# Kernel tuning notes

Measured on AMD Instinct MI355X. Metric: run time of the kernel, lower is better.

## Reference

```python
import jax, jax.numpy as jnp
import numpy as np

LAYERS, BLOCKS = 10, 4
RC, DC, SC, EC, CLASSES = 32, 32, 256, 256, 256
KS = 2
OUTPUT_LENGTH = 4096


def _dilations():
    ds = []
    init = 1
    for _b in range(BLOCKS):
        nd = 1
        for _i in range(LAYERS):
            ds.append((nd, init))
            init = nd
            nd *= 2
    return ds

DILATIONS = _dilations()


def dilate(x, dilation, init_dilation):
    # Faithful port of pytorch-wavenet dilate(): folds time into batch (or back)
    # by the ratio dilation/init_dilation, front-padding with zeros if needed.
    n, c, l = x.shape
    if dilation == init_dilation:
        return x
    if dilation > init_dilation:
        r = dilation // init_dilation
        new_l = -(-l // r) * r  # ceil to multiple of r
        if new_l != l:
            x = jnp.pad(x, ((0, 0), (0, 0), (new_l - l, 0)))  # pad_start=True
            l = new_l
        l_new, n_new = l // r, n * r
    else:
        r = init_dilation // dilation
        l_new, n_new = l * r, n // r
    x = jnp.transpose(x, (1, 2, 0)).reshape(c, l_new, n_new)  # (c, l, n) view
    return jnp.transpose(x, (2, 0, 1))


def conv2tap(x, w):
    # valid Conv1d, kernel_size=2, no bias; x: [n,c,l], w: [o,c,2]
    return jax.lax.conv_general_dilated(x, w, (1,), 'VALID',
                                        dimension_numbers=('NCH', 'OIH', 'NCH'))


def conv1x1(x, w):
    # 1x1 Conv1d as einsum; x: [n,c,l], w: [o,c]
    return jnp.einsum('ncl,oc->nol', x, w)


def setup_inputs() -> dict:
    key = jax.random.key(0)
    ks = jax.random.split(key, 10)
    nl = LAYERS * BLOCKS
    s = 0.05
    return {
        'x_input': jax.random.normal(ks[0], (8, CLASSES, 16384), jnp.float32),
        'start_w': jax.random.normal(ks[1], (RC, CLASSES, 1), jnp.float32) * s,
        'filter_w': jax.random.normal(ks[2], (nl, DC, RC, KS), jnp.float32) * s,
        'gate_w': jax.random.normal(ks[3], (nl, DC, RC, KS), jnp.float32) * s,
        'residual_w': jax.random.normal(ks[4], (nl, RC, DC, 1), jnp.float32) * s,
        'skip_w': jax.random.normal(ks[5], (nl, SC, DC, 1), jnp.float32) * s,
        'end1_w': jax.random.normal(ks[6], (EC, SC, 1), jnp.float32) * s,
        'end1_b': jnp.zeros((EC,), jnp.float32),
        'end2_w': jax.random.normal(ks[7], (CLASSES, EC, 1), jnp.float32) * s,
        'end2_b': jnp.zeros((CLASSES,), jnp.float32),
    }


def reference(x_input, start_w, filter_w, gate_w, residual_w, skip_w,
              end1_w, end1_b, end2_w, end2_b):
    x = conv1x1(x_input, start_w[:, :, 0])
    x_skip = None
    for i, (d, d0) in enumerate(DILATIONS):
        xr = dilate(x, d, d0)
        f = jnp.tanh(conv2tap(xr, filter_w[i]))
        g = jax.nn.sigmoid(conv2tap(xr, gate_w[i]))
        x = f * g
        xs = dilate(x, 1, d) if x.shape[2] != 1 else x
        # NOTE: the source never reassigns `skip`, so its try/except always
        # falls to the except branch and only the LAST layer's skip survives.
        x_skip = conv1x1(xs, skip_w[i][:, :, 0])
        x = conv1x1(x, residual_w[i][:, :, 0]) + xr[:, :, KS - 1:]
    y = jax.nn.relu(x_skip)
    y = jax.nn.relu(conv1x1(y, end1_w[:, :, 0]) + end1_b[None, :, None])
    y = conv1x1(y, end2_w[:, :, 0]) + end2_b[None, :, None]
    n, c, _l = y.shape
    y = y[:, :, -OUTPUT_LENGTH:]
    return jnp.transpose(y, (0, 2, 1)).reshape(n * OUTPUT_LENGTH, c)
```

## Files before the change

kernel.cpp:

```cpp
#include <hip/hip_runtime.h>
#include <hip/hip_bf16.h>
#include <math.h>


#define TS   8192
#define T0   8188
#define NB   8
#define RCH  32
#define CLS  256
#define TOUT 4096

#define OFF_WBLOB 0
#define OFF_ST    204800
#define OFF_SK    212992
#define OFF_E1T   221184
#define OFF_E2T   286720
#define OFF_XA    352256
#define OFF_XB    (OFF_XA + NB*RCH*TS)
#define OFF_H1    (OFF_XB + NB*RCH*TS)
#define OFF_E1    (OFF_H1 + NB*256*TOUT)

__device__ __forceinline__ float tanh_fast(float x) {
    float e = __expf(2.0f * x);
    return 1.0f - 2.0f / (e + 1.0f);
}
__device__ __forceinline__ float sigmoid_fast(float x) {
    return 1.0f / (1.0f + __expf(-x));
}

__global__ void repack_kernel(const float* __restrict__ start_w,
                              const float* __restrict__ filter_w,
                              const float* __restrict__ gate_w,
                              const float* __restrict__ residual_w,
                              const float* __restrict__ skip_w,
                              const float* __restrict__ end1_w,
                              const float* __restrict__ end2_w,
                              float* __restrict__ ws) {
    int id = blockIdx.x * 256 + threadIdx.x;
    if (id < 204800) {
        int l = id / 5120, r = id % 5120;
        float v;
        if (r < 4096) {
            const float* src = (r < 2048) ? filter_w : gate_w;
            int rr = r & 2047;
            int ic = rr >> 6, k = (rr >> 5) & 1, oc = rr & 31;
            v = src[((l * 32 + oc) * 32 + ic) * 2 + k];
        } else {
            int rr = r - 4096;
            int ic = rr >> 5, oc = rr & 31;
            v = residual_w[(l * 32 + oc) * 32 + ic];
        }
        ws[OFF_WBLOB + id] = v;
    } else if (id < 204800 + 8192) {
        int r = id - 204800;
        int ic = r >> 5, oc = r & 31;
        ws[OFF_ST + r] = start_w[oc * 256 + ic];
    } else if (id < 212992 + 8192) {
        int r = id - 212992;
        int dc = r >> 8, sc = r & 255;
        ws[OFF_SK + r] = skip_w[(39 * 256 + sc) * 32 + dc];
    } else if (id < 221184 + 65536) {
        int r = id - 221184;
        int sc = r >> 8, ec = r & 255;
        ws[OFF_E1T + r] = end1_w[ec * 256 + sc];
    } else if (id < 286720 + 65536) {
        int r = id - 286720;
        int ec = r >> 8, cc = r & 255;
        ws[OFF_E2T + r] = end2_w[cc * 256 + ec];
    }
}

__global__ __launch_bounds__(256) void start_kernel(const float* __restrict__ xin,
                                                    const float* __restrict__ st,
                                                    float* __restrict__ xout) {
    int t = blockIdx.x * 256 + threadIdx.x;
    int og = blockIdx.y;
    int b = blockIdx.z;
    if (t >= T0) return;
    const float* xi = xin + (size_t)b * 256 * 16384 + (16384 - T0) + t;
    const float* wb = st + og * 16;
    float acc[16];
#pragma unroll
    for (int c = 0; c < 16; c++) acc[c] = 0.f;
#pragma unroll 4
    for (int ic = 0; ic < 256; ic++) {
        float xv = xi[ic * 16384];
        const float* w = wb + ic * 32;
#pragma unroll
        for (int c = 0; c < 16; c++) acc[c] = fmaf(w[c], xv, acc[c]);
    }
    float* xo = xout + ((size_t)(b * RCH) + og * 16) * TS + t;
#pragma unroll
    for (int c = 0; c < 16; c++) xo[c * TS] = acc[c];
}

__global__ __launch_bounds__(256) void layer_kernel(const float* __restrict__ xin,
                                                    float* __restrict__ xout,
                                                    const float* __restrict__ wl,
                                                    int d, int Tout) {
    __shared__ float hs[32][64];
    int tx = threadIdx.x;
    int cg = __builtin_amdgcn_readfirstlane(threadIdx.y);
    int t  = blockIdx.x * 64 + tx;
    int b  = blockIdx.y;
    bool act = (t < Tout);

    const float* xi = xin + (size_t)(b * RCH) * TS + t;
    const float* wf = wl +        cg * 8;
    const float* wg = wl + 2048 + cg * 8;
    const float* wr = wl + 4096 + cg * 8;

    float accf[8], accg[8];
#pragma unroll
    for (int j = 0; j < 8; j++) { accf[j] = 0.f; accg[j] = 0.f; }

#pragma unroll 4
    for (int ic = 0; ic < 32; ic++) {
        float a = xi[ic * TS];
        float c = xi[ic * TS + d];
        const float* w0 = wf + ic * 64;
        const float* w1 = wg + ic * 64;
#pragma unroll
        for (int j = 0; j < 8; j++) accf[j] = fmaf(w0[j],      a, accf[j]);
#pragma unroll
        for (int j = 0; j < 8; j++) accf[j] = fmaf(w0[32 + j], c, accf[j]);
#pragma unroll
        for (int j = 0; j < 8; j++) accg[j] = fmaf(w1[j],      a, accg[j]);
#pragma unroll
        for (int j = 0; j < 8; j++) accg[j] = fmaf(w1[32 + j], c, accg[j]);
    }

#pragma unroll
    for (int j = 0; j < 8; j++)
        hs[cg * 8 + j][tx] = tanh_fast(accf[j]) * sigmoid_fast(accg[j]);
    __syncthreads();

    float accr[8];
#pragma unroll
    for (int j = 0; j < 8; j++) accr[j] = xi[(cg * 8 + j) * TS + d];
#pragma unroll 4
    for (int ic = 0; ic < 32; ic++) {
        float h = hs[ic][tx];
        const float* w = wr + ic * 32;
#pragma unroll
        for (int j = 0; j < 8; j++) accr[j] = fmaf(w[j], h, accr[j]);
    }

    if (act) {
        float* xo = xout + ((size_t)(b * RCH) + cg * 8) * TS + t;
#pragma unroll
        for (int j = 0; j < 8; j++) xo[j * TS] = accr[j];
    }
}

__global__ __launch_bounds__(256) void layer_last_kernel(const float* __restrict__ xin,
                                                         float* __restrict__ xout,
                                                         const float* __restrict__ wl,
                                                         int d, int Tout) {
    int tx = threadIdx.x;
    int cg = __builtin_amdgcn_readfirstlane(threadIdx.y);
    int t  = blockIdx.x * 64 + tx;
    int b  = blockIdx.y;
    if (t >= Tout) return;
    const float* xi = xin + (size_t)(b * RCH) * TS + t;
    const float* wf = wl +        cg * 8;
    const float* wg = wl + 2048 + cg * 8;

    float accf[8], accg[8];
#pragma unroll
    for (int j = 0; j < 8; j++) { accf[j] = 0.f; accg[j] = 0.f; }
#pragma unroll 4
    for (int ic = 0; ic < 32; ic++) {
        float a = xi[ic * TS];
        float c = xi[ic * TS + d];
        const float* w0 = wf + ic * 64;
        const float* w1 = wg + ic * 64;
#pragma unroll
        for (int j = 0; j < 8; j++) accf[j] = fmaf(w0[j],      a, accf[j]);
#pragma unroll
        for (int j = 0; j < 8; j++) accf[j] = fmaf(w0[32 + j], c, accf[j]);
#pragma unroll
        for (int j = 0; j < 8; j++) accg[j] = fmaf(w1[j],      a, accg[j]);
#pragma unroll
        for (int j = 0; j < 8; j++) accg[j] = fmaf(w1[32 + j], c, accg[j]);
    }
    float* xo = xout + ((size_t)(b * RCH) + cg * 8) * TS + t;
#pragma unroll
    for (int j = 0; j < 8; j++)
        xo[j * TS] = tanh_fast(accf[j]) * sigmoid_fast(accg[j]);
}

__global__ __launch_bounds__(256) void skip_kernel(const float* __restrict__ xin,
                                                   const float* __restrict__ sk,
                                                   float* __restrict__ h1) {
    int t = blockIdx.x * 256 + threadIdx.x;
    int sg = blockIdx.y;
    int b = blockIdx.z;
    const float* xi = xin + (size_t)(b * RCH) * TS + t;
    const float* wb = sk + sg * 32;
    float acc[32];
#pragma unroll
    for (int j = 0; j < 32; j++) acc[j] = 0.f;
#pragma unroll 4
    for (int dc = 0; dc < 32; dc++) {
        float xv = xi[dc * TS];
        const float* w = wb + dc * 256;
#pragma unroll
        for (int j = 0; j < 32; j++) acc[j] = fmaf(w[j], xv, acc[j]);
    }
    float* ho = h1 + ((size_t)(b * 256) + sg * 32) * TOUT + t;
#pragma unroll
    for (int j = 0; j < 32; j++) ho[j * TOUT] = fmaxf(acc[j], 0.f);
}

__global__ __launch_bounds__(256) void end1_kernel(const float* __restrict__ h1,
                                                   const float* __restrict__ e1t,
                                                   const float* __restrict__ b1,
                                                   float* __restrict__ e1) {
    int t = blockIdx.x * 256 + threadIdx.x;
    int eg = blockIdx.y;
    int b = blockIdx.z;
    const float* hp = h1 + (size_t)(b * 256) * TOUT + t;
    const float* wb = e1t + eg * 32;
    float acc[32];
#pragma unroll
    for (int j = 0; j < 32; j++) acc[j] = b1[eg * 32 + j];
#pragma unroll 4
    for (int sc = 0; sc < 256; sc++) {
        float xv = hp[sc * TOUT];
        const float* w = wb + sc * 256;
#pragma unroll
        for (int j = 0; j < 32; j++) acc[j] = fmaf(w[j], xv, acc[j]);
    }
    float* ep = e1 + ((size_t)(b * 256) + eg * 32) * TOUT + t;
#pragma unroll
    for (int j = 0; j < 32; j++) ep[j * TOUT] = fmaxf(acc[j], 0.f);
}

__global__ __launch_bounds__(256) void end2_kernel(const float* __restrict__ e1,
                                                   const float* __restrict__ e2t,
                                                   const float* __restrict__ b2,
                                                   float* __restrict__ out) {
    int t = blockIdx.x * 256 + threadIdx.x;
    int cg = blockIdx.y;
    int b = blockIdx.z;
    const float* ep = e1 + (size_t)(b * 256) * TOUT + t;
    const float* wb = e2t + cg * 32;
    float acc[32];
#pragma unroll
    for (int j = 0; j < 32; j++) acc[j] = b2[cg * 32 + j];
#pragma unroll 4
    for (int ec = 0; ec < 256; ec++) {
        float xv = ep[ec * TOUT];
        const float* w = wb + ec * 256;
#pragma unroll
        for (int j = 0; j < 32; j++) acc[j] = fmaf(w[j], xv, acc[j]);
    }
    float* op = out + ((size_t)(b * TOUT + t)) * CLS + cg * 32;
#pragma unroll
    for (int j = 0; j < 8; j++)
        ((float4*)op)[j] = make_float4(acc[4*j], acc[4*j+1], acc[4*j+2], acc[4*j+3]);
}

extern "C" void kernel_launch(void* const* d_in, const int* in_sizes, int n_in,
                              void* d_out, int out_size, void* d_ws, size_t ws_size,
                              hipStream_t stream) {
    const float* x_input    = (const float*)d_in[0];
    const float* start_w    = (const float*)d_in[1];
    const float* filter_w   = (const float*)d_in[2];
    const float* gate_w     = (const float*)d_in[3];
    const float* residual_w = (const float*)d_in[4];
    const float* skip_w     = (const float*)d_in[5];
    const float* end1_w     = (const float*)d_in[6];
    const float* end1_b     = (const float*)d_in[7];
    const float* end2_w     = (const float*)d_in[8];
    const float* end2_b     = (const float*)d_in[9];
    float* ws  = (float*)d_ws;
    float* out = (float*)d_out;

    repack_kernel<<<dim3((352256 + 255) / 256), 256, 0, stream>>>(
        start_w, filter_w, gate_w, residual_w, skip_w, end1_w, end2_w, ws);

    start_kernel<<<dim3(32, 2, NB), 256, 0, stream>>>(
        x_input, ws + OFF_ST, ws + OFF_XA);

    float* bufs[2] = { ws + OFF_XA, ws + OFF_XB };
    int cur = 0;
    int Tin = T0;
    int cnt = 0;
    for (int bl = 0; bl < 4; bl++) {
        int dd = 1;
        for (int i = 0; i < 10; i++) {
            int Tout_l = Tin - dd;
            dim3 grid((Tout_l + 63) / 64, NB);
            dim3 blk(64, 4);
            if (cnt < 39) {
                layer_kernel<<<grid, blk, 0, stream>>>(
                    bufs[cur], bufs[cur ^ 1], ws + OFF_WBLOB + (size_t)cnt * 5120, dd, Tout_l);
            } else {
                layer_last_kernel<<<grid, blk, 0, stream>>>(
                    bufs[cur], bufs[cur ^ 1], ws + OFF_WBLOB + (size_t)cnt * 5120, dd, Tout_l);
            }
            cur ^= 1;
            Tin = Tout_l;
            dd *= 2;
            cnt++;
        }
    }

    skip_kernel<<<dim3(16, 8, NB), 256, 0, stream>>>(bufs[cur], ws + OFF_SK, ws + OFF_H1);
    end1_kernel<<<dim3(16, 8, NB), 256, 0, stream>>>(ws + OFF_H1, ws + OFF_E1T, end1_b, ws + OFF_E1);
    end2_kernel<<<dim3(16, 8, NB), 256, 0, stream>>>(ws + OFF_E1, ws + OFF_E2T, end2_b, out);
}
```

Baseline: 910.1 us.

## Fuse five dilated layers per kernel using shared-memory halo tiles

Replaces 40 per-layer launches with 8 kernels, each running five consecutive dilated layers on a time tile kept in LDS with a 31-sample halo. Dilations 32..512 are handled by deinterleaving time with a stride of 32, so the second group of five layers again uses dilations 1..16. The goal is to remove global-memory round trips and launch overhead between layers. In exchange, the halo is recomputed, three 20KB LDS buffers per block limit occupancy, and the strided global gathers in fuse5_q are uncoalesced.

```diff
diff --git a/kernel.cpp b/kernel.cpp
--- a/kernel.cpp
+++ b/kernel.cpp
@@ -94,100 +94,123 @@
     for (int c = 0; c < 16; c++) xo[c * TS] = acc[c];
 }
 
-__global__ __launch_bounds__(256) void layer_kernel(const float* __restrict__ xin,
-                                                    float* __restrict__ xout,
-                                                    const float* __restrict__ wl,
-                                                    int d, int Tout) {
-    __shared__ float hs[32][64];
+__device__ __forceinline__ void run5(float (*B0)[160], float (*B1)[160],
+                                     float (*Hb)[160], const float* wl,
+                                     int E0, int tx, int cg, bool lastGrp) {
+    int E = E0;
+#pragma unroll 1
+    for (int j = 0; j < 5; j++) {
+        int d = 1 << j;
+        int L = E - d;
+        float (*Bin)[160]  = (j & 1) ? B1 : B0;
+        float (*Bout)[160] = (j & 1) ? B0 : B1;
+        const float* wf = wl +        cg * 8;
+        const float* wg = wl + 2048 + cg * 8;
+        const float* wr = wl + 4096 + cg * 8;
+
+        for (int p = tx; p < L; p += 64) {
+            float accf[8], accg[8];
+#pragma unroll
+            for (int o = 0; o < 8; o++) { accf[o] = 0.f; accg[o] = 0.f; }
+#pragma unroll 8
+            for (int ic = 0; ic < 32; ic++) {
+                float a = Bin[ic][p];
+                float c = Bin[ic][p + d];
+                const float* w0 = wf + ic * 64;
+                const float* w1 = wg + ic * 64;
+#pragma unroll
+                for (int o = 0; o < 8; o++) accf[o] = fmaf(w0[o],      a, accf[o]);
+#pragma unroll
+                for (int o = 0; o < 8; o++) accf[o] = fmaf(w0[32 + o], c, accf[o]);
+#pragma unroll
+                for (int o = 0; o < 8; o++) accg[o] = fmaf(w1[o],      a, accg[o]);
+#pragma unroll
+                for (int o = 0; o < 8; o++) accg[o] = fmaf(w1[32 + o], c, accg[o]);
+            }
+#pragma unroll
+            for (int o = 0; o < 8; o++)
+                Hb[cg * 8 + o][p] = tanh_fast(accf[o]) * sigmoid_fast(accg[o]);
+        }
+        __syncthreads();
+
+        if (lastGrp && j == 4) {
+            for (int p = tx; p < L; p += 64)
+#pragma unroll
+                for (int o = 0; o < 8; o++) Bout[cg * 8 + o][p] = Hb[cg * 8 + o][p];
+        } else {
+            for (int p = tx; p < L; p += 64) {
+                float acc[8];
+#pragma unroll
+                for (int o = 0; o < 8; o++) acc[o] = Bin[cg * 8 + o][p + d];
+#pragma unroll 8
+                for (int ic = 0; ic < 32; ic++) {
+                    float hv = Hb[ic][p];
+#pragma unroll
+                    for (int o = 0; o < 8; o++) acc[o] = fmaf(wr[ic * 32 + o], hv, acc[o]);
+                }
+#pragma unroll
+                for (int o = 0; o < 8; o++) Bout[cg * 8 + o][p] = acc[o];
+            }
+        }
+        __syncthreads();
+        E = L;
+        wl += 5120;
+    }
+}
+
+__global__ __launch_bounds__(256) void fuse5_t(const float* __restrict__ xin,
+                                               float* __restrict__ xout,
+                                               const float* __restrict__ wl0,
+                                               int T_in, int T_a) {
+    __shared__ float B0[32][160], B1[32][160], Hb[32][160];
     int tx = threadIdx.x;
     int cg = __builtin_amdgcn_readfirstlane(threadIdx.y);
-    int t  = blockIdx.x * 64 + tx;
+    int tid = threadIdx.y * 64 + tx;
+    int t0 = blockIdx.x * 128;
     int b  = blockIdx.y;
-    bool act = (t < Tout);
-
-    const float* xi = xin + (size_t)(b * RCH) * TS + t;
-    const float* wf = wl +        cg * 8;
-    const float* wg = wl + 2048 + cg * 8;
-    const float* wr = wl + 4096 + cg * 8;
-
-    float accf[8], accg[8];
-#pragma unroll
-    for (int j = 0; j < 8; j++) { accf[j] = 0.f; accg[j] = 0.f; }
-
-#pragma unroll 4
-    for (int ic = 0; ic < 32; ic++) {
-        float a = xi[ic * TS];
-        float c = xi[ic * TS + d];
-        const float* w0 = wf + ic * 64;
-        const float* w1 = wg + ic * 64;
-#pragma unroll
-        for (int j = 0; j < 8; j++) accf[j] = fmaf(w0[j],      a, accf[j]);
-#pragma unroll
-        for (int j = 0; j < 8; j++) accf[j] = fmaf(w0[32 + j], c, accf[j]);
-#pragma unroll
-        for (int j = 0; j < 8; j++) accg[j] = fmaf(w1[j],      a, accg[j]);
-#pragma unroll
-        for (int j = 0; j < 8; j++) accg[j] = fmaf(w1[32 + j], c, accg[j]);
-    }
-
-#pragma unroll
-    for (int j = 0; j < 8; j++)
-        hs[cg * 8 + j][tx] = tanh_fast(accf[j]) * sigmoid_fast(accg[j]);
+    int E0 = min(159, T_in - t0);
+    const float* xr = xin + (size_t)(b * 32) * TS + t0;
+#pragma unroll 4
+    for (int ch = 0; ch < 32; ch++)
+        if (tid < E0) B0[ch][tid] = xr[(size_t)ch * TS + tid];
     __syncthreads();
 
-    float accr[8];
-#pragma unroll
-    for (int j = 0; j < 8; j++) accr[j] = xi[(cg * 8 + j) * TS + d];
-#pragma unroll 4
-    for (int ic = 0; ic < 32; ic++) {
-        float h = hs[ic][tx];
-        const float* w = wr + ic * 32;
-#pragma unroll
-        for (int j = 0; j < 8; j++) accr[j] = fmaf(w[j], h, accr[j]);
-    }
-
-    if (act) {
-        float* xo = xout + ((size_t)(b * RCH) + cg * 8) * TS + t;
-#pragma unroll
-        for (int j = 0; j < 8; j++) xo[j * TS] = accr[j];
-    }
-}
-
-__global__ __launch_bounds__(256) void layer_last_kernel(const float* __restrict__ xin,
-                                                         float* __restrict__ xout,
-                                                         const float* __restrict__ wl,
-                                                         int d, int Tout) {
+    run5(B0, B1, Hb, wl0, E0, tx, cg, false);
+
+    int valid = min(128, T_a - t0);
+    float* xo = xout + (size_t)(b * 32) * TS + t0;
+#pragma unroll 4
+    for (int ch = 0; ch < 32; ch++)
+        if (tid < valid) xo[(size_t)ch * TS + tid] = B1[ch][tid];
+}
+
+__global__ __launch_bounds__(256) void fuse5_q(const float* __restrict__ yin,
+                                               float* __restrict__ zout,
+                                               const float* __restrict__ wl0,
+                                               int T_b, int T_z, int lastGrp) {
+    __shared__ float B0[32][160], B1[32][160], Hb[32][160];
     int tx = threadIdx.x;
     int cg = __builtin_amdgcn_readfirstlane(threadIdx.y);
-    int t  = blockIdx.x * 64 + tx;
-    int b  = blockIdx.y;
-    if (t >= Tout) return;
-    const float* xi = xin + (size_t)(b * RCH) * TS + t;
-    const float* wf = wl +        cg * 8;
-    const float* wg = wl + 2048 + cg * 8;
-
-    float accf[8], accg[8];
-#pragma unroll
-    for (int j = 0; j < 8; j++) { accf[j] = 0.f; accg[j] = 0.f; }
-#pragma unroll 4
-    for (int ic = 0; ic < 32; ic++) {
-        float a = xi[ic * TS];
-        float c = xi[ic * TS + d];
-        const float* w0 = wf + ic * 64;
-        const float* w1 = wg + ic * 64;
-#pragma unroll
-        for (int j = 0; j < 8; j++) accf[j] = fmaf(w0[j],      a, accf[j]);
-#pragma unroll
-        for (int j = 0; j < 8; j++) accf[j] = fmaf(w0[32 + j], c, accf[j]);
-#pragma unroll
-        for (int j = 0; j < 8; j++) accg[j] = fmaf(w1[j],      a, accg[j]);
-#pragma unroll
-        for (int j = 0; j < 8; j++) accg[j] = fmaf(w1[32 + j], c, accg[j]);
-    }
-    float* xo = xout + ((size_t)(b * RCH) + cg * 8) * TS + t;
-#pragma unroll
-    for (int j = 0; j < 8; j++)
-        xo[j * TS] = tanh_fast(accf[j]) * sigmoid_fast(accg[j]);
+    int tid = threadIdx.y * 64 + tx;
+    int q0 = blockIdx.x * 128;
+    int r  = blockIdx.y;
+    int b  = blockIdx.z;
+    int Qr = (T_b - r + 31) >> 5;
+    int E0 = min(159, Qr - q0);
+    const float* yb = yin + (size_t)(b * 32) * TS + r;
+#pragma unroll 4
+    for (int ch = 0; ch < 32; ch++)
+        if (tid < E0) B0[ch][tid] = yb[(size_t)ch * TS + ((q0 + tid) << 5)];
+    __syncthreads();
+
+    run5(B0, B1, Hb, wl0, E0, tx, cg, lastGrp != 0);
+
+    int Qz = (T_z - r + 31) >> 5;
+    int valid = min(128, Qz - q0);
+    float* zb = zout + (size_t)(b * 32) * TS + r;
+#pragma unroll 4
+    for (int ch = 0; ch < 32; ch++)
+        if (tid < valid) zb[(size_t)ch * TS + ((q0 + tid) << 5)] = B1[ch][tid];
 }
 
 __global__ __launch_bounds__(256) void skip_kernel(const float* __restrict__ xin,
@@ -284,28 +307,24 @@
     start_kernel<<<dim3(32, 2, NB), 256, 0, stream>>>(
         x_input, ws + OFF_ST, ws + OFF_XA);
 
+    const int Tin_g[4] = { 8188, 7165, 6142, 5119 };
+    const int Ta_g[4]  = { 8157, 7134, 6111, 5088 };
+    const int Tz_g[4]  = { 7165, 6142, 5119, 4096 };
+
     float* bufs[2] = { ws + OFF_XA, ws + OFF_XB };
     int cur = 0;
-    int Tin = T0;
-    int cnt = 0;
-    for (int bl = 0; bl < 4; bl++) {
-        int dd = 1;
-        for (int i = 0; i < 10; i++) {
-            int Tout_l = Tin - dd;
-            dim3 grid((Tout_l + 63) / 64, NB);
-            dim3 blk(64, 4);
-            if (cnt < 39) {
-                layer_kernel<<<grid, blk, 0, stream>>>(
-                    bufs[cur], bufs[cur ^ 1], ws + OFF_WBLOB + (size_t)cnt * 5120, dd, Tout_l);
-            } else {
-                layer_last_kernel<<<grid, blk, 0, stream>>>(
-                    bufs[cur], bufs[cur ^ 1], ws + OFF_WBLOB + (size_t)cnt * 5120, dd, Tout_l);
-            }
-            cur ^= 1;
-            Tin = Tout_l;
-            dd *= 2;
-            cnt++;
-        }
+    for (int g = 0; g < 4; g++) {
+        int gxA = (Ta_g[g] + 127) / 128;
+        fuse5_t<<<dim3(gxA, NB), dim3(64, 4), 0, stream>>>(
+            bufs[cur], bufs[cur ^ 1], ws + OFF_WBLOB + (size_t)(g * 10) * 5120,
+            Tin_g[g], Ta_g[g]);
+        cur ^= 1;
+        int Qz = (Tz_g[g] + 31) / 32;
+        int gxB = (Qz + 127) / 128;
+        fuse5_q<<<dim3(gxB, 32, NB), dim3(64, 4), 0, stream>>>(
+            bufs[cur], bufs[cur ^ 1], ws + OFF_WBLOB + (size_t)(g * 10 + 5) * 5120,
+            Ta_g[g], Tz_g[g], g == 3);
+        cur ^= 1;
     }
 
     skip_kernel<<<dim3(16, 8, NB), 256, 0, stream>>>(bufs[cur], ws + OFF_SK, ws + OFF_H1);
```

Result: slower. 1.165 ms (+28.0%).

## Stage input tiles in shared memory and widen blocks to 512 threads

Applied to the files above, without the earlier changes.

All kernels now cooperatively load a 32-channel by 64-timestep input tile into LDS. Each block then has 8 waves sharing that tile, each computing a smaller output-channel group, instead of every thread re-reading strided global memory per channel. The layer kernel also reuses the staged shifted tile for the residual add, and the last-layer variant is folded in behind a flag. Trade-offs are more syncs, more LDS per block, and for the end convolutions more output per block (all 256 channels) but fewer blocks in flight.

```diff
diff --git a/kernel.cpp b/kernel.cpp
--- a/kernel.cpp
+++ b/kernel.cpp
@@ -70,191 +70,213 @@
     }
 }
 
-__global__ __launch_bounds__(256) void start_kernel(const float* __restrict__ xin,
+__global__ __launch_bounds__(512) void start_kernel(const float* __restrict__ xin,
                                                     const float* __restrict__ st,
                                                     float* __restrict__ xout) {
-    int t = blockIdx.x * 256 + threadIdx.x;
-    int og = blockIdx.y;
-    int b = blockIdx.z;
-    if (t >= T0) return;
-    const float* xi = xin + (size_t)b * 256 * 16384 + (16384 - T0) + t;
-    const float* wb = st + og * 16;
-    float acc[16];
-#pragma unroll
-    for (int c = 0; c < 16; c++) acc[c] = 0.f;
-#pragma unroll 4
-    for (int ic = 0; ic < 256; ic++) {
-        float xv = xi[ic * 16384];
-        const float* w = wb + ic * 32;
-#pragma unroll
-        for (int c = 0; c < 16; c++) acc[c] = fmaf(w[c], xv, acc[c]);
-    }
-    float* xo = xout + ((size_t)(b * RCH) + og * 16) * TS + t;
-#pragma unroll
-    for (int c = 0; c < 16; c++) xo[c * TS] = acc[c];
-}
-
-__global__ __launch_bounds__(256) void layer_kernel(const float* __restrict__ xin,
+    __shared__ float S[32][64];
+    int tx = threadIdx.x, ty = threadIdx.y;
+    int cg = __builtin_amdgcn_readfirstlane(ty);
+    int tid = ty * 64 + tx;
+    int t0 = blockIdx.x * 64;
+    int b  = blockIdx.y;
+    int t  = t0 + tx;
+    const float* xb = xin + (size_t)b * 256 * 16384 + (16384 - T0);
+    float acc[4] = {0.f, 0.f, 0.f, 0.f};
+    for (int k0 = 0; k0 < 256; k0 += 32) {
+        if (k0) __syncthreads();
+        for (int i = tid; i < 2048; i += 512) {
+            int ic = i >> 6, tt = i & 63;
+            int tg = t0 + tt;
+            S[ic][tt] = (tg < T0) ? xb[(size_t)(k0 + ic) * 16384 + tg] : 0.f;
+        }
+        __syncthreads();
+        const float* wbase = st + (size_t)k0 * 32 + cg * 4;
+#pragma unroll 8
+        for (int i = 0; i < 32; i++) {
+            float xv = S[i][tx];
+            const float* w = wbase + i * 32;
+#pragma unroll
+            for (int o = 0; o < 4; o++) acc[o] = fmaf(w[o], xv, acc[o]);
+        }
+    }
+    if (t < T0) {
+        float* xo = xout + ((size_t)(b * RCH) + cg * 4) * TS + t;
+#pragma unroll
+        for (int o = 0; o < 4; o++) xo[o * TS] = acc[o];
+    }
+}
+
+__global__ __launch_bounds__(512) void layer_kernel(const float* __restrict__ xin,
                                                     float* __restrict__ xout,
                                                     const float* __restrict__ wl,
-                                                    int d, int Tout) {
-    __shared__ float hs[32][64];
-    int tx = threadIdx.x;
-    int cg = __builtin_amdgcn_readfirstlane(threadIdx.y);
-    int t  = blockIdx.x * 64 + tx;
-    int b  = blockIdx.y;
-    bool act = (t < Tout);
-
-    const float* xi = xin + (size_t)(b * RCH) * TS + t;
-    const float* wf = wl +        cg * 8;
-    const float* wg = wl + 2048 + cg * 8;
-    const float* wr = wl + 4096 + cg * 8;
-
-    float accf[8], accg[8];
-#pragma unroll
-    for (int j = 0; j < 8; j++) { accf[j] = 0.f; accg[j] = 0.f; }
-
-#pragma unroll 4
+                                                    int d, int Tout, int last) {
+    __shared__ float A[32][64], C[32][64], Hs[32][64];
+    int tx = threadIdx.x, ty = threadIdx.y;
+    int cg = __builtin_amdgcn_readfirstlane(ty);
+    int tid = ty * 64 + tx;
+    int t0 = blockIdx.x * 64;
+    int b  = blockIdx.y;
+    int t  = t0 + tx;
+    const float* xb = xin + (size_t)(b * RCH) * TS;
+    for (int i = tid; i < 2048; i += 512) {
+        int ch = i >> 6, tt = i & 63;
+        A[ch][tt] = xb[(size_t)ch * TS + t0 + tt];
+        C[ch][tt] = xb[(size_t)ch * TS + t0 + d + tt];
+    }
+    __syncthreads();
+
+    const float* wf = wl +        cg * 4;
+    const float* wg = wl + 2048 + cg * 4;
+    const float* wr = wl + 4096 + cg * 4;
+
+    float accf[4] = {0.f, 0.f, 0.f, 0.f}, accg[4] = {0.f, 0.f, 0.f, 0.f};
+#pragma unroll 8
     for (int ic = 0; ic < 32; ic++) {
-        float a = xi[ic * TS];
-        float c = xi[ic * TS + d];
+        float a = A[ic][tx];
+        float c = C[ic][tx];
         const float* w0 = wf + ic * 64;
         const float* w1 = wg + ic * 64;
 #pragma unroll
-        for (int j = 0; j < 8; j++) accf[j] = fmaf(w0[j],      a, accf[j]);
-#pragma unroll
-        for (int j = 0; j < 8; j++) accf[j] = fmaf(w0[32 + j], c, accf[j]);
-#pragma unroll
-        for (int j = 0; j < 8; j++) accg[j] = fmaf(w1[j],      a, accg[j]);
-#pragma unroll
-        for (int j = 0; j < 8; j++) accg[j] = fmaf(w1[32 + j], c, accg[j]);
-    }
-
-#pragma unroll
-    for (int j = 0; j < 8; j++)
-        hs[cg * 8 + j][tx] = tanh_fast(accf[j]) * sigmoid_fast(accg[j]);
+        for (int o = 0; o < 4; o++) accf[o] = fmaf(w0[o],      a, accf[o]);
+#pragma unroll
+        for (int o = 0; o < 4; o++) accf[o] = fmaf(w0[32 + o], c, accf[o]);
+#pragma unroll
+        for (int o = 0; o < 4; o++) accg[o] = fmaf(w1[o],      a, accg[o]);
+#pragma unroll
+        for (int o = 0; o < 4; o++) accg[o] = fmaf(w1[32 + o], c, accg[o]);
+    }
+
+    float h[4];
+#pragma unroll
+    for (int o = 0; o < 4; o++) h[o] = tanh_fast(accf[o]) * sigmoid_fast(accg[o]);
+
+    if (last) {
+        if (t < Tout) {
+            float* xo = xout + ((size_t)(b * RCH) + cg * 4) * TS + t;
+#pragma unroll
+            for (int o = 0; o < 4; o++) xo[o * TS] = h[o];
+        }
+        return;
+    }
+
+#pragma unroll
+    for (int o = 0; o < 4; o++) Hs[cg * 4 + o][tx] = h[o];
     __syncthreads();
 
-    float accr[8];
-#pragma unroll
-    for (int j = 0; j < 8; j++) accr[j] = xi[(cg * 8 + j) * TS + d];
-#pragma unroll 4
+    float acc[4];
+#pragma unroll
+    for (int o = 0; o < 4; o++) acc[o] = C[cg * 4 + o][tx];
+#pragma unroll 8
     for (int ic = 0; ic < 32; ic++) {
-        float h = hs[ic][tx];
-        const float* w = wr + ic * 32;
-#pragma unroll
-        for (int j = 0; j < 8; j++) accr[j] = fmaf(w[j], h, accr[j]);
-    }
-
-    if (act) {
-        float* xo = xout + ((size_t)(b * RCH) + cg * 8) * TS + t;
-#pragma unroll
-        for (int j = 0; j < 8; j++) xo[j * TS] = accr[j];
-    }
-}
-
-__global__ __launch_bounds__(256) void layer_last_kernel(const float* __restrict__ xin,
-                                                         float* __restrict__ xout,
-                                                         const float* __restrict__ wl,
-                                                         int d, int Tout) {
-    int tx = threadIdx.x;
-    int cg = __builtin_amdgcn_readfirstlane(threadIdx.y);
-    int t  = blockIdx.x * 64 + tx;
-    int b  = blockIdx.y;
-    if (t >= Tout) return;
-    const float* xi = xin + (size_t)(b * RCH) * TS + t;
-    const float* wf = wl +        cg * 8;
-    const float* wg = wl + 2048 + cg * 8;
-
-    float accf[8], accg[8];
-#pragma unroll
-    for (int j = 0; j < 8; j++) { accf[j] = 0.f; accg[j] = 0.f; }
-#pragma unroll 4
-    for (int ic = 0; ic < 32; ic++) {
-        float a = xi[ic * TS];
-        float c = xi[ic * TS + d];
-        const float* w0 = wf + ic * 64;
-        const float* w1 = wg + ic * 64;
-#pragma unroll
-        for (int j = 0; j < 8; j++) accf[j] = fmaf(w0[j],      a, accf[j]);
-#pragma unroll
-        for (int j = 0; j < 8; j++) accf[j] = fmaf(w0[32 + j], c, accf[j]);
-#pragma unroll
-        for (int j = 0; j < 8; j++) accg[j] = fmaf(w1[j],      a, accg[j]);
-#pragma unroll
-        for (int j = 0; j < 8; j++) accg[j] = fmaf(w1[32 + j], c, accg[j]);
-    }
-    float* xo = xout + ((size_t)(b * RCH) + cg * 8) * TS + t;
-#pragma unroll
-    for (int j = 0; j < 8; j++)
-        xo[j * TS] = tanh_fast(accf[j]) * sigmoid_fast(accg[j]);
-}
-
-__global__ __launch_bounds__(256) void skip_kernel(const float* __restrict__ xin,
+        float hv = Hs[ic][tx];
+#pragma unroll
+        for (int o = 0; o < 4; o++) acc[o] = fmaf(wr[ic * 32 + o], hv, acc[o]);
+    }
+    if (t < Tout) {
+        float* xo = xout + ((size_t)(b * RCH) + cg * 4) * TS + t;
+#pragma unroll
+        for (int o = 0; o < 4; o++) xo[o * TS] = acc[o];
+    }
+}
+
+__global__ __launch_bounds__(512) void skip_kernel(const float* __restrict__ xin,
                                                    const float* __restrict__ sk,
                                                    float* __restrict__ h1) {
-    int t = blockIdx.x * 256 + threadIdx.x;
-    int sg = blockIdx.y;
-    int b = blockIdx.z;
-    const float* xi = xin + (size_t)(b * RCH) * TS + t;
-    const float* wb = sk + sg * 32;
+    __shared__ float S[32][64];
+    int tx = threadIdx.x, ty = threadIdx.y;
+    int cg = __builtin_amdgcn_readfirstlane(ty);
+    int tid = ty * 64 + tx;
+    int t0 = blockIdx.x * 64;
+    int b  = blockIdx.y;
+    int t  = t0 + tx;
+    const float* xb = xin + (size_t)(b * RCH) * TS;
+    for (int i = tid; i < 2048; i += 512) {
+        int ch = i >> 6, tt = i & 63;
+        S[ch][tt] = xb[(size_t)ch * TS + t0 + tt];
+    }
+    __syncthreads();
+    const float* wb = sk + cg * 32;
     float acc[32];
 #pragma unroll
     for (int j = 0; j < 32; j++) acc[j] = 0.f;
 #pragma unroll 4
     for (int dc = 0; dc < 32; dc++) {
-        float xv = xi[dc * TS];
+        float xv = S[dc][tx];
         const float* w = wb + dc * 256;
 #pragma unroll
         for (int j = 0; j < 32; j++) acc[j] = fmaf(w[j], xv, acc[j]);
     }
-    float* ho = h1 + ((size_t)(b * 256) + sg * 32) * TOUT + t;
+    float* ho = h1 + ((size_t)(b * 256) + cg * 32) * TOUT + t;
 #pragma unroll
     for (int j = 0; j < 32; j++) ho[j * TOUT] = fmaxf(acc[j], 0.f);
 }
 
-__global__ __launch_bounds__(256) void end1_kernel(const float* __restrict__ h1,
+__global__ __launch_bounds__(512) void end1_kernel(const float* __restrict__ h1,
                                                    const float* __restrict__ e1t,
                                                    const float* __restrict__ b1,
                                                    float* __restrict__ e1) {
-    int t = blockIdx.x * 256 + threadIdx.x;
-    int eg = blockIdx.y;
-    int b = blockIdx.z;
-    const float* hp = h1 + (size_t)(b * 256) * TOUT + t;
-    const float* wb = e1t + eg * 32;
+    __shared__ float S[32][64];
+    int tx = threadIdx.x, ty = threadIdx.y;
+    int cg = __builtin_amdgcn_readfirstlane(ty);
+    int tid = ty * 64 + tx;
+    int t0 = blockIdx.x * 64;
+    int b  = blockIdx.y;
+    int t  = t0 + tx;
+    const float* hp = h1 + (size_t)(b * 256) * TOUT;
+    const float* wb = e1t + cg * 32;
     float acc[32];
 #pragma unroll
-    for (int j = 0; j < 32; j++) acc[j] = b1[eg * 32 + j];
+    for (int j = 0; j < 32; j++) acc[j] = b1[cg * 32 + j];
+    for (int k0 = 0; k0 < 256; k0 += 32) {
+        if (k0) __syncthreads();
+        for (int i = tid; i < 2048; i += 512) {
+            int sc = i >> 6, tt = i & 63;
+            S[sc][tt] = hp[(size_t)(k0 + sc) * TOUT + t0 + tt];
+        }
+        __syncthreads();
 #pragma unroll 4
-    for (int sc = 0; sc < 256; sc++) {
-        float xv = hp[sc * TOUT];
-        const float* w = wb + sc * 256;
-#pragma unroll
-        for (int j = 0; j < 32; j++) acc[j] = fmaf(w[j], xv, acc[j]);
-    }
-    float* ep = e1 + ((size_t)(b * 256) + eg * 32) * TOUT + t;
+        for (int sc = 0; sc < 32; sc++) {
+            float xv = S[sc][tx];
+            const float* w = wb + (size_t)(k0 + sc) * 256;
+#pragma unroll
+            for (int j = 0; j < 32; j++) acc[j] = fmaf(w[j], xv, acc[j]);
+        }
+    }
+    float* ep = e1 + ((size_t)(b * 256) + cg * 32) * TOUT + t;
 #pragma unroll
     for (int j = 0; j < 32; j++) ep[j * TOUT] = fmaxf(acc[j], 0.f);
 }
 
-__global__ __launch_bounds__(256) void end2_kernel(const float* __restrict__ e1,
+__global__ __launch_bounds__(512) void end2_kernel(const float* __restrict__ e1,
                                                    const float* __restrict__ e2t,
                                                    const float* __restrict__ b2,
                                                    float* __restrict__ out) {
-    int t = blockIdx.x * 256 + threadIdx.x;
-    int cg = blockIdx.y;
-    int b = blockIdx.z;
-    const float* ep = e1 + (size_t)(b * 256) * TOUT + t;
+    __shared__ float S[32][64];
+    int tx = threadIdx.x, ty = threadIdx.y;
+    int cg = __builtin_amdgcn_readfirstlane(ty);
+    int tid = ty * 64 + tx;
+    int t0 = blockIdx.x * 64;
+    int b  = blockIdx.y;
+    int t  = t0 + tx;
+    const float* ep = e1 + (size_t)(b * 256) * TOUT;
     const float* wb = e2t + cg * 32;
     float acc[32];
 #pragma unroll
     for (int j = 0; j < 32; j++) acc[j] = b2[cg * 32 + j];
+    for (int k0 = 0; k0 < 256; k0 += 32) {
+        if (k0) __syncthreads();
+        for (int i = tid; i < 2048; i += 512) {
+            int ec = i >> 6, tt = i & 63;
+            S[ec][tt] = ep[(size_t)(k0 + ec) * TOUT + t0 + tt];
+        }
+        __syncthreads();
 #pragma unroll 4
-    for (int ec = 0; ec < 256; ec++) {
-        float xv = ep[ec * TOUT];
-        const float* w = wb + ec * 256;
-#pragma unroll
-        for (int j = 0; j < 32; j++) acc[j] = fmaf(w[j], xv, acc[j]);
+        for (int ec = 0; ec < 32; ec++) {
+            float xv = S[ec][tx];
+            const float* w = wb + (size_t)(k0 + ec) * 256;
+#pragma unroll
+            for (int j = 0; j < 32; j++) acc[j] = fmaf(w[j], xv, acc[j]);
+        }
     }
     float* op = out + ((size_t)(b * TOUT + t)) * CLS + cg * 32;
 #pragma unroll
@@ -281,7 +303,7 @@
     repack_kernel<<<dim3((352256 + 255) / 256), 256, 0, stream>>>(
         start_w, filter_w, gate_w, residual_w, skip_w, end1_w, end2_w, ws);
 
-    start_kernel<<<dim3(32, 2, NB), 256, 0, stream>>>(
+    start_kernel<<<dim3(128, NB), dim3(64, 8), 0, stream>>>(
         x_input, ws + OFF_ST, ws + OFF_XA);
 
     float* bufs[2] = { ws + OFF_XA, ws + OFF_XB };
@@ -292,15 +314,9 @@
         int dd = 1;
         for (int i = 0; i < 10; i++) {
             int Tout_l = Tin - dd;
-            dim3 grid((Tout_l + 63) / 64, NB);
-            dim3 blk(64, 4);
-            if (cnt < 39) {
-                layer_kernel<<<grid, blk, 0, stream>>>(
-                    bufs[cur], bufs[cur ^ 1], ws + OFF_WBLOB + (size_t)cnt * 5120, dd, Tout_l);
-            } else {
-                layer_last_kernel<<<grid, blk, 0, stream>>>(
-                    bufs[cur], bufs[cur ^ 1], ws + OFF_WBLOB + (size_t)cnt * 5120, dd, Tout_l);
-            }
+            layer_kernel<<<dim3((Tout_l + 63) / 64, NB), dim3(64, 8), 0, stream>>>(
+                bufs[cur], bufs[cur ^ 1], ws + OFF_WBLOB + (size_t)cnt * 5120,
+                dd, Tout_l, cnt == 39);
             cur ^= 1;
             Tin = Tout_l;
             dd *= 2;
@@ -308,7 +324,7 @@
         }
     }
 
-    skip_kernel<<<dim3(16, 8, NB), 256, 0, stream>>>(bufs[cur], ws + OFF_SK, ws + OFF_H1);
-    end1_kernel<<<dim3(16, 8, NB), 256, 0, stream>>>(ws + OFF_H1, ws + OFF_E1T, end1_b, ws + OFF_E1);
-    end2_kernel<<<dim3(16, 8, NB), 256, 0, stream>>>(ws + OFF_E1, ws + OFF_E2T, end2_b, out);
-}
+    skip_kernel<<<dim3(64, NB), dim3(64, 8), 0, stream>>>(bufs[cur], ws + OFF_SK, ws + OFF_H1);
+    end1_kernel<<<dim3(64, NB), dim3(64, 8), 0, stream>>>(ws + OFF_H1, ws + OFF_E1T, end1_b, ws + OFF_E1);
+    end2_kernel<<<dim3(64, NB), dim3(64, 8), 0, stream>>>(ws + OFF_E1, ws + OFF_E2T, end2_b, out);
+}
```

Result: slower. 953.9 us (+4.8%).
